# Performance work log

Measured on AMD Instinct MI355X. Metric: run time of the kernel, lower is better.

Reference implementation:

```python
import math
import jax, jax.numpy as jnp
import numpy as np

FACTOR = 5


def setup_inputs() -> dict:
    key = jax.random.key(0)
    kq, kk, kv, ki = jax.random.split(key, 4)
    B, H, L, D = 4, 8, 2048, 64
    sample_k = min(FACTOR * math.ceil(math.log(L)), L)  # 40
    queries = jax.random.normal(kq, (B, H, L, D), dtype=jnp.float32)
    keys = jax.random.normal(kk, (B, H, L, D), dtype=jnp.float32)
    values = jax.random.normal(kv, (B, H, L, D), dtype=jnp.float32)
    index_sample = jax.random.randint(ki, (L, sample_k), 0, L, dtype=jnp.int64 if jax.config.jax_enable_x64 else jnp.int32)
    return {"queries": queries, "keys": keys, "values": values, "index_sample": index_sample}


def reference(queries, keys, values, index_sample):
    B, H, L_Q, D = queries.shape
    L_K = keys.shape[2]
    u = min(FACTOR * math.ceil(math.log(L_Q)), L_Q)  # n_top queries (= 40)
    scale = 1.0 / math.sqrt(D)

    # --- _prob_QK: sparsity measurement over randomly sampled keys ---
    # K_sample[b,h,q,s,:] = keys[b,h,index_sample[q,s],:]  -> [B,H,L_Q,S,D]
    K_sample = keys[:, :, index_sample, :]
    Q_K_sample = jnp.einsum('bhqd,bhqsd->bhqs', queries, K_sample)  # [B,H,L_Q,S]
    M = Q_K_sample.max(axis=-1) - Q_K_sample.sum(axis=-1) / L_K      # [B,H,L_Q]
    _, M_top = jax.lax.top_k(M, u)                                    # [B,H,u]

    Q_reduce = jnp.take_along_axis(queries, M_top[..., None], axis=2)  # [B,H,u,D]
    scores_top = jnp.einsum('bhud,bhkd->bhuk', Q_reduce, keys) * scale  # [B,H,u,L_K]

    # --- initial context: causal cumulative sum of V (mask_flag=True) ---
    context = jnp.cumsum(values, axis=2)  # [B,H,L_Q,D]

    # --- ProbMask: causal rows gathered at the selected query indices ---
    causal = jnp.triu(jnp.ones((L_Q, L_K), dtype=bool), 1)  # [L_Q,L_K]
    mask = causal[M_top]                                     # [B,H,u,L_K]
    scores_top = jnp.where(mask, -jnp.inf, scores_top)

    attn = jax.nn.softmax(scores_top, axis=-1)                       # [B,H,u,L_K]
    update = jnp.einsum('bhuk,bhkd->bhud', attn, values)             # [B,H,u,D]

    b_idx = jnp.arange(B)[:, None, None]
    h_idx = jnp.arange(H)[None, :, None]
    context = context.at[b_idx, h_idx, M_top].set(update.astype(context.dtype))
    return context
```

## Files before the change

kernel.cpp:

```cpp
#include <hip/hip_runtime.h>
#include <math.h>

#define BB 4
#define HH 8
#define LL 2048
#define DD 64
#define SK 40
#define BH (BB*HH)
#define NC 16
#define CK 128

__device__ __forceinline__ unsigned ordu(float v) {
    unsigned u = __float_as_uint(v);
    return (u & 0x80000000u) ? ~u : (u | 0x80000000u);
}

__device__ __forceinline__ float dot4(float4 a, float4 b) {
    return a.x * b.x + a.y * b.y + a.z * b.z + a.w * b.w;
}

__global__ __launch_bounds__(256) void stage1_kernel(
        const float* __restrict__ Q, const float* __restrict__ K,
        const float* __restrict__ V, const int* __restrict__ IDX,
        float* __restrict__ M, float* __restrict__ csum) {
    int tid = threadIdx.x;
    if (blockIdx.x < 1024) {
        int x = blockIdx.x;
        int bhLo = x & 7;
        int r = x >> 3;
        int bhHi = r & 3;
        int chunk = r >> 2;
        int bh = bhHi * 8 + bhLo;
        int qbase = chunk * 64;
        int w = tid >> 6, lane = tid & 63;
        int qw = lane >> 2, c = lane & 3;
        int qi = w * 16 + qw;
        int qpos = qbase + qi;

        __shared__ int sidx[64 * SK];
        for (int i = tid; i < 64 * SK; i += 256) sidx[i] = IDX[(size_t)qbase * SK + i];

        const float4* Q4 = (const float4*)Q;
        const float4* K4 = (const float4*)K;
        float4 qreg[4];
        #pragma unroll
        for (int j = 0; j < 4; ++j)
            qreg[j] = Q4[((size_t)bh * LL + qpos) * 16 + j * 4 + c];
        __syncthreads();

        size_t kb4 = (size_t)bh * LL * 16;
        float mx = -INFINITY, sm = 0.f;

        float4 ka[4], kb[4];
        {
            const float4* kr = K4 + kb4 + (size_t)sidx[qi * SK] * 16;
            #pragma unroll
            for (int j = 0; j < 4; ++j) ka[j] = kr[j * 4 + c];
        }
        for (int s = 0; s < SK; s += 2) {
            {
                const float4* kr = K4 + kb4 + (size_t)sidx[qi * SK + s + 1] * 16;
                #pragma unroll
                for (int j = 0; j < 4; ++j) kb[j] = kr[j * 4 + c];
            }
            {
                float p = dot4(qreg[0], ka[0]) + dot4(qreg[1], ka[1])
                        + dot4(qreg[2], ka[2]) + dot4(qreg[3], ka[3]);
                p += __shfl_xor(p, 1, 64);
                p += __shfl_xor(p, 2, 64);
                mx = fmaxf(mx, p);
                sm += p;
            }
            if (s + 2 < SK) {
                const float4* kr = K4 + kb4 + (size_t)sidx[qi * SK + s + 2] * 16;
                #pragma unroll
                for (int j = 0; j < 4; ++j) ka[j] = kr[j * 4 + c];
            }
            {
                float p = dot4(qreg[0], kb[0]) + dot4(qreg[1], kb[1])
                        + dot4(qreg[2], kb[2]) + dot4(qreg[3], kb[3]);
                p += __shfl_xor(p, 1, 64);
                p += __shfl_xor(p, 2, 64);
                mx = fmaxf(mx, p);
                sm += p;
            }
        }
        if (c == 0) M[(size_t)bh * LL + qpos] = mx - sm * (1.0f / (float)LL);
    } else {
        int x = blockIdx.x - 1024;
        int bhLo = x & 7, r = x >> 3;
        int bhHi = r & 3, c = r >> 2;
        int bh = bhHi * 8 + bhLo;
        int d = tid & 63, sg = tid >> 6;
        size_t base = (size_t)bh * LL * DD;
        int row0 = c * 128 + sg * 32;
        float s = 0.f;
        for (int j = 0; j < 32; ++j) s += V[base + (size_t)(row0 + j) * DD + d];
        __shared__ float part[4][DD];
        part[sg][d] = s;
        __syncthreads();
        if (sg == 0)
            csum[((size_t)bh * 16 + c) * DD + d] = part[0][d] + part[1][d] + part[2][d] + part[3][d];
    }
}

__global__ __launch_bounds__(256) void radix_kernel(
        const float* __restrict__ M, int* __restrict__ topk) {
    int tid = threadIdx.x;
    int bh = blockIdx.x;
    __shared__ unsigned hist[256];
    __shared__ unsigned sfx[256];
    __shared__ unsigned bc_prefix, bc_need;
    __shared__ unsigned cnt_gt, cnt_eq;
    __shared__ int eqlist[128];

    unsigned v[8];
    #pragma unroll
    for (int j = 0; j < 8; ++j)
        v[j] = ordu(M[(size_t)bh * LL + tid + j * 256]);

    unsigned prefix = 0, need = SK;
    #pragma unroll
    for (int pass = 0; pass < 4; ++pass) {
        const int s = 24 - 8 * pass;
        const unsigned maskHigh = (pass == 0) ? 0u : (0xFFFFFFFFu << (s + 8));
        hist[tid] = 0;
        __syncthreads();
        #pragma unroll
        for (int j = 0; j < 8; ++j)
            if (((v[j] ^ prefix) & maskHigh) == 0)
                atomicAdd(&hist[(v[j] >> s) & 0xFF], 1u);
        __syncthreads();
        sfx[tid] = hist[tid];
        __syncthreads();
        #pragma unroll
        for (int off = 1; off < 256; off <<= 1) {
            unsigned t = (tid + off < 256) ? sfx[tid + off] : 0u;
            __syncthreads();
            sfx[tid] += t;
            __syncthreads();
        }
        unsigned above = (tid < 255) ? sfx[tid + 1] : 0u;
        if (above < need && sfx[tid] >= need) {
            bc_prefix = prefix | ((unsigned)tid << s);
            bc_need = need - above;
        }
        __syncthreads();
        prefix = bc_prefix;
        need = bc_need;
        __syncthreads();
    }
    unsigned T = prefix;
    if (tid == 0) { cnt_gt = 0; cnt_eq = 0; }
    __syncthreads();
    #pragma unroll
    for (int j = 0; j < 8; ++j) {
        int idx = tid + j * 256;
        if (v[j] > T) { unsigned p = atomicAdd(&cnt_gt, 1u); topk[bh * SK + p] = idx; }
        else if (v[j] == T) { unsigned p = atomicAdd(&cnt_eq, 1u); if (p < 128) eqlist[p] = idx; }
    }
    __syncthreads();
    if (tid == 0) {
        int ne = (int)min(cnt_eq, 128u);
        unsigned base = cnt_gt;
        for (unsigned r2 = 0; r2 < need; ++r2) {
            int bj = 0, bv = 0x7FFFFFFF;
            for (int j = 0; j < ne; ++j)
                if (eqlist[j] < bv) { bv = eqlist[j]; bj = j; }
            topk[bh * SK + base + r2] = bv;
            eqlist[bj] = 0x7FFFFFFF;
        }
    }
}

__global__ __launch_bounds__(256) void attn_cumsum_kernel(
        const float* __restrict__ Q, const float* __restrict__ K,
        const float* __restrict__ V, const int* __restrict__ topk,
        const float* __restrict__ csum, float* __restrict__ out,
        float* __restrict__ pm, float* __restrict__ pl,
        float* __restrict__ po) {
    int tid = threadIdx.x;
    __shared__ int qp[SK];
    __shared__ float4 sq4[SK][16];
    __shared__ float SC[CK][SK + 1];
    __shared__ float part[4][DD];

    if (blockIdx.x < 512) {
        int x = blockIdx.x;
        int bhLo = x & 7;
        int r = x >> 3;
        int c = r & 15;
        int bhHi = r >> 4;
        int bh = bhHi * 8 + bhLo;
        int w = tid >> 6, lane = tid & 63;
        int cbase = c * CK;

        if (tid < SK) qp[tid] = topk[bh * SK + tid];
        __syncthreads();
        const float4* Q4 = (const float4*)Q;
        const float4* K4 = (const float4*)K;
        const float4* V4 = (const float4*)V;
        for (int i = tid; i < SK * 16; i += 256) {
            int u = i >> 4, j = i & 15;
            sq4[u][j] = Q4[((size_t)bh * LL + qp[u]) * 16 + j];
        }
        __syncthreads();

        {
            int half = tid & 1;
            int kk = tid >> 1;
            int kg = cbase + kk;
            size_t kb4 = (size_t)bh * LL * 16;
            float4 kreg[8];
            const float4* kr = K4 + kb4 + (size_t)kg * 16 + half * 8;
            #pragma unroll
            for (int j = 0; j < 8; ++j) kreg[j] = kr[j];
            #pragma unroll 4
            for (int u = 0; u < SK; ++u) {
                int qpu = qp[u];
                if (cbase > qpu) {
                    if (half == 0) SC[kk][u] = -INFINITY;
                    continue;
                }
                float pa = 0.f, pb = 0.f;
                #pragma unroll
                for (int j = 0; j < 4; ++j) {
                    float4 qv = sq4[u][half * 8 + j];
                    pa += kreg[j].x * qv.x + kreg[j].y * qv.y + kreg[j].z * qv.z + kreg[j].w * qv.w;
                }
                #pragma unroll
                for (int j = 4; j < 8; ++j) {
                    float4 qv = sq4[u][half * 8 + j];
                    pb += kreg[j].x * qv.x + kreg[j].y * qv.y + kreg[j].z * qv.z + kreg[j].w * qv.w;
                }
                float p = pa + pb;
                p += __shfl_xor(p, 1, 64);
                if (half == 0) SC[kk][u] = (kg <= qpu) ? p * 0.125f : -INFINITY;
            }
        }
        __syncthreads();

        for (int u = w; u < SK; u += 4) {
            float s0 = SC[lane][u], s1 = SC[lane + 64][u];
            float m = fmaxf(s0, s1);
            #pragma unroll
            for (int off = 32; off > 0; off >>= 1) m = fmaxf(m, __shfl_xor(m, off, 64));
            float e0 = 0.f, e1 = 0.f;
            if (m != -INFINITY) {
                e0 = expf(s0 - m);
                e1 = expf(s1 - m);
            }
            SC[lane][u] = e0;
            SC[lane + 64][u] = e1;
            float ls = e0 + e1;
            #pragma unroll
            for (int off = 32; off > 0; off >>= 1) ls += __shfl_xor(ls, off, 64);
            if (lane == 0) {
                size_t pb = (size_t)(bh * SK + u) * NC + c;
                pm[pb] = m;
                pl[pb] = ls;
            }
        }
        __syncthreads();

        {
            int ks = tid & 3;
            int dg = (tid >> 2) & 15;
            int ug = tid >> 6;
            int u0 = ug * 10;
            float4 acc[10];
            #pragma unroll
            for (int i = 0; i < 10; ++i) acc[i] = make_float4(0.f, 0.f, 0.f, 0.f);
            for (int t = 0; t < CK / 4; ++t) {
                int k = t * 4 + ks;
                float4 vv = V4[((size_t)bh * LL + cbase + k) * 16 + dg];
                #pragma unroll
                for (int i = 0; i < 10; ++i) {
                    float pw = SC[k][u0 + i];
                    acc[i].x += pw * vv.x; acc[i].y += pw * vv.y;
                    acc[i].z += pw * vv.z; acc[i].w += pw * vv.w;
                }
            }
            #pragma unroll
            for (int i = 0; i < 10; ++i) {
                acc[i].x += __shfl_xor(acc[i].x, 1, 64); acc[i].x += __shfl_xor(acc[i].x, 2, 64);
                acc[i].y += __shfl_xor(acc[i].y, 1, 64); acc[i].y += __shfl_xor(acc[i].y, 2, 64);
                acc[i].z += __shfl_xor(acc[i].z, 1, 64); acc[i].z += __shfl_xor(acc[i].z, 2, 64);
                acc[i].w += __shfl_xor(acc[i].w, 1, 64); acc[i].w += __shfl_xor(acc[i].w, 2, 64);
            }
            if (ks == 0) {
                #pragma unroll
                for (int i = 0; i < 10; ++i) {
                    float4* dst = (float4*)&po[((size_t)(bh * SK + u0 + i) * NC + c) * DD + dg * 4];
                    *dst = acc[i];
                }
            }
        }
    } else {
        int x = blockIdx.x - 512;
        int bhLo = x & 7, r = x >> 3;
        int bhHi = r & 3, c = r >> 2;
        int bh = bhHi * 8 + bhLo;
        int d = tid & 63, sg = tid >> 6;
        size_t base = (size_t)bh * LL * DD;
        int row0 = c * 128 + sg * 32;
        float v[32];
        #pragma unroll
        for (int j = 0; j < 32; ++j) v[j] = V[base + (size_t)(row0 + j) * DD + d];
        float s = 0.f;
        #pragma unroll
        for (int j = 0; j < 32; ++j) s += v[j];
        part[sg][d] = s;
        __syncthreads();
        float pre = 0.f;
        for (int cc = 0; cc < c; ++cc) pre += csum[((size_t)bh * 16 + cc) * DD + d];
        for (int ss = 0; ss < sg; ++ss) pre += part[ss][d];
        float acc = pre;
        #pragma unroll
        for (int j = 0; j < 32; ++j) {
            acc += v[j];
            out[base + (size_t)(row0 + j) * DD + d] = acc;
        }
    }
}

__global__ __launch_bounds__(256) void combine_kernel(
        const float* __restrict__ pm, const float* __restrict__ pl,
        const float* __restrict__ po, const int* __restrict__ topk,
        float* __restrict__ out) {
    int g = blockIdx.x * 4 + (threadIdx.x >> 6);
    int d = threadIdx.x & 63;
    int qpos = topk[g];
    int bh = g / SK;
    size_t gb = (size_t)g * NC;
    float gm = -INFINITY;
    #pragma unroll
    for (int j = 0; j < NC; ++j) gm = fmaxf(gm, pm[gb + j]);
    float L = 0.f, o = 0.f;
    #pragma unroll
    for (int j = 0; j < NC; ++j) {
        float pmj = pm[gb + j];
        float wj = (pmj == -INFINITY) ? 0.f : expf(pmj - gm);
        L += pl[gb + j] * wj;
        o += po[(gb + j) * DD + d] * wj;
    }
    out[((size_t)bh * LL + qpos) * DD + d] = o / L;
}

extern "C" void kernel_launch(void* const* d_in, const int* in_sizes, int n_in,
                              void* d_out, int out_size, void* d_ws, size_t ws_size,
                              hipStream_t stream) {
    const float* Q   = (const float*)d_in[0];
    const float* K   = (const float*)d_in[1];
    const float* V   = (const float*)d_in[2];
    const int*   IDX = (const int*)d_in[3];
    float* out = (float*)d_out;

    char* ws = (char*)d_ws;
    float* M    = (float*)ws;  ws += (size_t)BH * LL * sizeof(float);
    int*   topk = (int*)ws;    ws += ((size_t)BH * SK * sizeof(int) + 255) & ~255ull;
    float* csum = (float*)ws;  ws += (size_t)BH * 16 * DD * sizeof(float);
    float* pm   = (float*)ws;  ws += ((size_t)BH * SK * NC * sizeof(float) + 255) & ~255ull;
    float* pl   = (float*)ws;  ws += ((size_t)BH * SK * NC * sizeof(float) + 255) & ~255ull;
    float* po   = (float*)ws;

    stage1_kernel<<<1536, 256, 0, stream>>>(Q, K, V, IDX, M, csum);
    radix_kernel<<<32, 256, 0, stream>>>(M, topk);
    attn_cumsum_kernel<<<1024, 256, 0, stream>>>(Q, K, V, topk, csum, out, pm, pl, po);
    combine_kernel<<<320, 256, 0, stream>>>(pm, pl, po, topk, out);
}
```

Measured before the change: 157.9 us.

## Fold radix top-k into attention blocks and merge stage1 work per block

Removes the separate radix top-k launch: each of the 512 attention blocks recomputes the top-k selection for its (b,h) from M in shared memory, sorts the indices by position, and chunk 0 writes them out for the combine kernel. Stage1 now runs 512 blocks, each scoring two heads that share the same sampled key indices and also doing one V column-sum chunk, in place of 1536 specialised blocks. This saves a kernel launch and its serial dependency and reuses sidx loads across heads, but the radix selection is now repeated 16 times per head and stage1 blocks carry more registers and work.

```diff
diff --git a/kernel.cpp b/kernel.cpp
--- a/kernel.cpp
+++ b/kernel.cpp
@@ -24,166 +24,115 @@
         const float* __restrict__ V, const int* __restrict__ IDX,
         float* __restrict__ M, float* __restrict__ csum) {
     int tid = threadIdx.x;
-    if (blockIdx.x < 1024) {
-        int x = blockIdx.x;
-        int bhLo = x & 7;
-        int r = x >> 3;
-        int bhHi = r & 3;
-        int chunk = r >> 2;
-        int bh = bhHi * 8 + bhLo;
-        int qbase = chunk * 64;
-        int w = tid >> 6, lane = tid & 63;
-        int qw = lane >> 2, c = lane & 3;
-        int qi = w * 16 + qw;
-        int qpos = qbase + qi;
-
-        __shared__ int sidx[64 * SK];
-        for (int i = tid; i < 64 * SK; i += 256) sidx[i] = IDX[(size_t)qbase * SK + i];
-
-        const float4* Q4 = (const float4*)Q;
-        const float4* K4 = (const float4*)K;
-        float4 qreg[4];
-        #pragma unroll
-        for (int j = 0; j < 4; ++j)
-            qreg[j] = Q4[((size_t)bh * LL + qpos) * 16 + j * 4 + c];
-        __syncthreads();
-
-        size_t kb4 = (size_t)bh * LL * 16;
-        float mx = -INFINITY, sm = 0.f;
-
-        float4 ka[4], kb[4];
-        {
-            const float4* kr = K4 + kb4 + (size_t)sidx[qi * SK] * 16;
-            #pragma unroll
-            for (int j = 0; j < 4; ++j) ka[j] = kr[j * 4 + c];
-        }
-        for (int s = 0; s < SK; s += 2) {
-            {
-                const float4* kr = K4 + kb4 + (size_t)sidx[qi * SK + s + 1] * 16;
-                #pragma unroll
-                for (int j = 0; j < 4; ++j) kb[j] = kr[j * 4 + c];
-            }
-            {
-                float p = dot4(qreg[0], ka[0]) + dot4(qreg[1], ka[1])
-                        + dot4(qreg[2], ka[2]) + dot4(qreg[3], ka[3]);
-                p += __shfl_xor(p, 1, 64);
-                p += __shfl_xor(p, 2, 64);
-                mx = fmaxf(mx, p);
-                sm += p;
-            }
-            if (s + 2 < SK) {
-                const float4* kr = K4 + kb4 + (size_t)sidx[qi * SK + s + 2] * 16;
-                #pragma unroll
-                for (int j = 0; j < 4; ++j) ka[j] = kr[j * 4 + c];
-            }
-            {
-                float p = dot4(qreg[0], kb[0]) + dot4(qreg[1], kb[1])
-                        + dot4(qreg[2], kb[2]) + dot4(qreg[3], kb[3]);
-                p += __shfl_xor(p, 1, 64);
-                p += __shfl_xor(p, 2, 64);
-                mx = fmaxf(mx, p);
-                sm += p;
-            }
-        }
-        if (c == 0) M[(size_t)bh * LL + qpos] = mx - sm * (1.0f / (float)LL);
-    } else {
-        int x = blockIdx.x - 1024;
-        int bhLo = x & 7, r = x >> 3;
-        int bhHi = r & 3, c = r >> 2;
-        int bh = bhHi * 8 + bhLo;
+    int b = blockIdx.x;
+    int bhLo = b & 7;
+    int bhA = bhLo + 8 * ((b >> 3) & 1);
+    int bhB = bhA + 16;
+    int chunk = b >> 4;
+    int qbase = chunk * 64;
+    int w = tid >> 6, lane = tid & 63;
+    int qw = lane >> 2, c = lane & 3;
+    int qi = w * 16 + qw;
+    int qpos = qbase + qi;
+
+    __shared__ int sidx[64 * SK];
+    __shared__ float part[4][DD];
+
+    for (int i = tid; i < 64 * SK; i += 256) sidx[i] = IDX[(size_t)qbase * SK + i];
+
+    const float4* Q4 = (const float4*)Q;
+    const float4* K4 = (const float4*)K;
+    float4 qA[4], qB[4];
+    #pragma unroll
+    for (int j = 0; j < 4; ++j) {
+        qA[j] = Q4[((size_t)bhA * LL + qpos) * 16 + j * 4 + c];
+        qB[j] = Q4[((size_t)bhB * LL + qpos) * 16 + j * 4 + c];
+    }
+    __syncthreads();
+
+    size_t kbA = (size_t)bhA * LL * 16;
+    size_t kbB = (size_t)bhB * LL * 16;
+    float mxA = -INFINITY, smA = 0.f, mxB = -INFINITY, smB = 0.f;
+
+    float4 a0[4], b0[4], a1[4], b1[4];
+    {
+        int ks = sidx[qi * SK];
+        const float4* krA = K4 + kbA + (size_t)ks * 16;
+        const float4* krB = K4 + kbB + (size_t)ks * 16;
+        #pragma unroll
+        for (int j = 0; j < 4; ++j) { a0[j] = krA[j * 4 + c]; b0[j] = krB[j * 4 + c]; }
+    }
+    for (int s = 0; s < SK; s += 2) {
+        {
+            int ks = sidx[qi * SK + s + 1];
+            const float4* krA = K4 + kbA + (size_t)ks * 16;
+            const float4* krB = K4 + kbB + (size_t)ks * 16;
+            #pragma unroll
+            for (int j = 0; j < 4; ++j) { a1[j] = krA[j * 4 + c]; b1[j] = krB[j * 4 + c]; }
+        }
+        {
+            float pA = dot4(qA[0], a0[0]) + dot4(qA[1], a0[1])
+                     + dot4(qA[2], a0[2]) + dot4(qA[3], a0[3]);
+            float pB = dot4(qB[0], b0[0]) + dot4(qB[1], b0[1])
+                     + dot4(qB[2], b0[2]) + dot4(qB[3], b0[3]);
+            pA += __shfl_xor(pA, 1, 64); pA += __shfl_xor(pA, 2, 64);
+            pB += __shfl_xor(pB, 1, 64); pB += __shfl_xor(pB, 2, 64);
+            mxA = fmaxf(mxA, pA); smA += pA;
+            mxB = fmaxf(mxB, pB); smB += pB;
+        }
+        if (s + 2 < SK) {
+            int ks = sidx[qi * SK + s + 2];
+            const float4* krA = K4 + kbA + (size_t)ks * 16;
+            const float4* krB = K4 + kbB + (size_t)ks * 16;
+            #pragma unroll
+            for (int j = 0; j < 4; ++j) { a0[j] = krA[j * 4 + c]; b0[j] = krB[j * 4 + c]; }
+        }
+        {
+            float pA = dot4(qA[0], a1[0]) + dot4(qA[1], a1[1])
+                     + dot4(qA[2], a1[2]) + dot4(qA[3], a1[3]);
+            float pB = dot4(qB[0], b1[0]) + dot4(qB[1], b1[1])
+                     + dot4(qB[2], b1[2]) + dot4(qB[3], b1[3]);
+            pA += __shfl_xor(pA, 1, 64); pA += __shfl_xor(pA, 2, 64);
+            pB += __shfl_xor(pB, 1, 64); pB += __shfl_xor(pB, 2, 64);
+            mxA = fmaxf(mxA, pA); smA += pA;
+            mxB = fmaxf(mxB, pB); smB += pB;
+        }
+    }
+    if (c == 0) {
+        M[(size_t)bhA * LL + qpos] = mxA - smA * (1.0f / (float)LL);
+        M[(size_t)bhB * LL + qpos] = mxB - smB * (1.0f / (float)LL);
+    }
+
+    {
+        int bhv = (b & 7) + 8 * ((b >> 3) & 3);
+        int cv = b >> 5;
         int d = tid & 63, sg = tid >> 6;
-        size_t base = (size_t)bh * LL * DD;
-        int row0 = c * 128 + sg * 32;
-        float s = 0.f;
-        for (int j = 0; j < 32; ++j) s += V[base + (size_t)(row0 + j) * DD + d];
-        __shared__ float part[4][DD];
-        part[sg][d] = s;
+        size_t base = (size_t)bhv * LL * DD;
+        int row0 = cv * 128 + sg * 32;
+        float s2 = 0.f;
+        for (int j = 0; j < 32; ++j) s2 += V[base + (size_t)(row0 + j) * DD + d];
+        part[sg][d] = s2;
         __syncthreads();
         if (sg == 0)
-            csum[((size_t)bh * 16 + c) * DD + d] = part[0][d] + part[1][d] + part[2][d] + part[3][d];
-    }
-}
-
-__global__ __launch_bounds__(256) void radix_kernel(
-        const float* __restrict__ M, int* __restrict__ topk) {
-    int tid = threadIdx.x;
-    int bh = blockIdx.x;
-    __shared__ unsigned hist[256];
-    __shared__ unsigned sfx[256];
-    __shared__ unsigned bc_prefix, bc_need;
-    __shared__ unsigned cnt_gt, cnt_eq;
-    __shared__ int eqlist[128];
-
-    unsigned v[8];
-    #pragma unroll
-    for (int j = 0; j < 8; ++j)
-        v[j] = ordu(M[(size_t)bh * LL + tid + j * 256]);
-
-    unsigned prefix = 0, need = SK;
-    #pragma unroll
-    for (int pass = 0; pass < 4; ++pass) {
-        const int s = 24 - 8 * pass;
-        const unsigned maskHigh = (pass == 0) ? 0u : (0xFFFFFFFFu << (s + 8));
-        hist[tid] = 0;
-        __syncthreads();
-        #pragma unroll
-        for (int j = 0; j < 8; ++j)
-            if (((v[j] ^ prefix) & maskHigh) == 0)
-                atomicAdd(&hist[(v[j] >> s) & 0xFF], 1u);
-        __syncthreads();
-        sfx[tid] = hist[tid];
-        __syncthreads();
-        #pragma unroll
-        for (int off = 1; off < 256; off <<= 1) {
-            unsigned t = (tid + off < 256) ? sfx[tid + off] : 0u;
-            __syncthreads();
-            sfx[tid] += t;
-            __syncthreads();
-        }
-        unsigned above = (tid < 255) ? sfx[tid + 1] : 0u;
-        if (above < need && sfx[tid] >= need) {
-            bc_prefix = prefix | ((unsigned)tid << s);
-            bc_need = need - above;
-        }
-        __syncthreads();
-        prefix = bc_prefix;
-        need = bc_need;
-        __syncthreads();
-    }
-    unsigned T = prefix;
-    if (tid == 0) { cnt_gt = 0; cnt_eq = 0; }
-    __syncthreads();
-    #pragma unroll
-    for (int j = 0; j < 8; ++j) {
-        int idx = tid + j * 256;
-        if (v[j] > T) { unsigned p = atomicAdd(&cnt_gt, 1u); topk[bh * SK + p] = idx; }
-        else if (v[j] == T) { unsigned p = atomicAdd(&cnt_eq, 1u); if (p < 128) eqlist[p] = idx; }
-    }
-    __syncthreads();
-    if (tid == 0) {
-        int ne = (int)min(cnt_eq, 128u);
-        unsigned base = cnt_gt;
-        for (unsigned r2 = 0; r2 < need; ++r2) {
-            int bj = 0, bv = 0x7FFFFFFF;
-            for (int j = 0; j < ne; ++j)
-                if (eqlist[j] < bv) { bv = eqlist[j]; bj = j; }
-            topk[bh * SK + base + r2] = bv;
-            eqlist[bj] = 0x7FFFFFFF;
-        }
+            csum[((size_t)bhv * 16 + cv) * DD + d] =
+                part[0][d] + part[1][d] + part[2][d] + part[3][d];
     }
 }
 
 __global__ __launch_bounds__(256) void attn_cumsum_kernel(
         const float* __restrict__ Q, const float* __restrict__ K,
-        const float* __restrict__ V, const int* __restrict__ topk,
+        const float* __restrict__ V, const float* __restrict__ M,
         const float* __restrict__ csum, float* __restrict__ out,
         float* __restrict__ pm, float* __restrict__ pl,
-        float* __restrict__ po) {
+        float* __restrict__ po, int* __restrict__ topk) {
     int tid = threadIdx.x;
     __shared__ int qp[SK];
     __shared__ float4 sq4[SK][16];
     __shared__ float SC[CK][SK + 1];
     __shared__ float part[4][DD];
+    __shared__ unsigned hist[256], sfx[256];
+    __shared__ int eqlist[128], qtmp[SK];
+    __shared__ unsigned bc_prefix, bc_need, cnt_gt, cnt_eq;
 
     if (blockIdx.x < 512) {
         int x = blockIdx.x;
@@ -195,8 +144,73 @@
         int w = tid >> 6, lane = tid & 63;
         int cbase = c * CK;
 
-        if (tid < SK) qp[tid] = topk[bh * SK + tid];
-        __syncthreads();
+        unsigned v[8];
+        #pragma unroll
+        for (int j = 0; j < 8; ++j)
+            v[j] = ordu(M[(size_t)bh * LL + tid + j * 256]);
+
+        unsigned prefix = 0, need = SK;
+        #pragma unroll
+        for (int pass = 0; pass < 4; ++pass) {
+            const int s = 24 - 8 * pass;
+            const unsigned maskHigh = (pass == 0) ? 0u : (0xFFFFFFFFu << (s + 8));
+            hist[tid] = 0;
+            __syncthreads();
+            #pragma unroll
+            for (int j = 0; j < 8; ++j)
+                if (((v[j] ^ prefix) & maskHigh) == 0)
+                    atomicAdd(&hist[(v[j] >> s) & 0xFF], 1u);
+            __syncthreads();
+            sfx[tid] = hist[tid];
+            __syncthreads();
+            #pragma unroll
+            for (int off = 1; off < 256; off <<= 1) {
+                unsigned t = (tid + off < 256) ? sfx[tid + off] : 0u;
+                __syncthreads();
+                sfx[tid] += t;
+                __syncthreads();
+            }
+            unsigned above = (tid < 255) ? sfx[tid + 1] : 0u;
+            if (above < need && sfx[tid] >= need) {
+                bc_prefix = prefix | ((unsigned)tid << s);
+                bc_need = need - above;
+            }
+            __syncthreads();
+            prefix = bc_prefix;
+            need = bc_need;
+            __syncthreads();
+        }
+        unsigned T = prefix;
+        if (tid == 0) { cnt_gt = 0; cnt_eq = 0; }
+        __syncthreads();
+        #pragma unroll
+        for (int j = 0; j < 8; ++j) {
+            int idx = tid + j * 256;
+            if (v[j] > T) { unsigned p = atomicAdd(&cnt_gt, 1u); qtmp[p] = idx; }
+            else if (v[j] == T) { unsigned p = atomicAdd(&cnt_eq, 1u); if (p < 128) eqlist[p] = idx; }
+        }
+        __syncthreads();
+        if (tid == 0) {
+            int ne = (int)min(cnt_eq, 128u);
+            unsigned base = cnt_gt;
+            for (unsigned r2 = 0; r2 < need; ++r2) {
+                int bj = 0, bv = 0x7FFFFFFF;
+                for (int j = 0; j < ne; ++j)
+                    if (eqlist[j] < bv) { bv = eqlist[j]; bj = j; }
+                qtmp[base + r2] = bv;
+                eqlist[bj] = 0x7FFFFFFF;
+            }
+        }
+        __syncthreads();
+        if (tid < SK) {
+            int mine = qtmp[tid];
+            int rank = 0;
+            for (int j = 0; j < SK; ++j) rank += (qtmp[j] < mine);
+            qp[rank] = mine;
+        }
+        __syncthreads();
+        if (c == 0 && tid < SK) topk[bh * SK + tid] = qp[tid];
+
         const float4* Q4 = (const float4*)Q;
         const float4* K4 = (const float4*)K;
         const float4* V4 = (const float4*)V;
@@ -364,8 +378,7 @@
     float* pl   = (float*)ws;  ws += ((size_t)BH * SK * NC * sizeof(float) + 255) & ~255ull;
     float* po   = (float*)ws;
 
-    stage1_kernel<<<1536, 256, 0, stream>>>(Q, K, V, IDX, M, csum);
-    radix_kernel<<<32, 256, 0, stream>>>(M, topk);
-    attn_cumsum_kernel<<<1024, 256, 0, stream>>>(Q, K, V, topk, csum, out, pm, pl, po);
+    stage1_kernel<<<512, 256, 0, stream>>>(Q, K, V, IDX, M, csum);
+    attn_cumsum_kernel<<<1024, 256, 0, stream>>>(Q, K, V, M, csum, out, pm, pl, po, topk);
     combine_kernel<<<320, 256, 0, stream>>>(pm, pl, po, topk, out);
 }
```

New measurement: 157.9 us. No clear change (+0.0%).
